# Kernel optimization log

Hardware: AMD Instinct MI355X
Metric: run time of the kernel (lower is better)

Reference implementation:

```python
import jax, jax.numpy as jnp
import numpy as np

N_NODES = 10000
N_EDGES = 640000
EMB_DIM = 128
NUM_RELS = 500


def setup_inputs() -> dict:
    key = jax.random.key(0)
    k_h, k_s, k_d, k_e, k_f, k_r = jax.random.split(key, 6)
    h = jax.random.normal(k_h, (N_NODES, EMB_DIM), dtype=jnp.float32)
    src = jax.random.randint(k_s, (N_EDGES,), 0, N_NODES, dtype=jnp.int64)
    dst = jax.random.randint(k_d, (N_EDGES,), 0, N_NODES, dtype=jnp.int64)
    etype = jax.random.randint(k_e, (N_EDGES,), 0, NUM_RELS, dtype=jnp.int64)
    fwd_rel = jax.random.normal(k_f, (NUM_RELS, EMB_DIM), dtype=jnp.float32)
    rev_rel = jax.random.normal(k_r, (NUM_RELS, EMB_DIM), dtype=jnp.float32)
    return {"h": h, "src": src, "dst": dst, "etype": etype,
            "fwd_rel": fwd_rel, "rev_rel": rev_rel}


def reference(h, src, dst, etype, fwd_rel, rev_rel):
    # DistMult forward-direction scoring (num_rels > 1 branch):
    #   w  = fwd_rel[etype]                  -> [E, D]
    #   ht = h[src] * w                      (u_mul_e)
    #   score[e] = <ht[e], h[dst[e]]>        (e_dot_v)
    w = fwd_rel[etype]                       # [E, D] gather
    h_u = h[src]                             # [E, D] gather
    h_v = h[dst]                             # [E, D] gather
    score = jnp.einsum("ed,ed,ed->e", h_u, w, h_v)  # [E]
    return score
```

## Files before the change

### kernel.cpp

```cpp
#include <hip/hip_runtime.h>
#include <hip/hip_fp16.h>


typedef unsigned short u16;

constexpr int EMB_DIM  = 128;
constexpr int MAX_RELS = 500;
constexpr int BLOCKS   = 256;
constexpr int THREADS  = 1024;

__global__ __launch_bounds__(256) void convert_fp16_kernel(
    const float* __restrict__ a, u16* __restrict__ a16, int n_a8,
    const float* __restrict__ b, u16* __restrict__ b16, int n_b8)
{
    const int total = n_a8 + n_b8;
    for (int i = blockIdx.x * blockDim.x + threadIdx.x; i < total;
         i += gridDim.x * blockDim.x) {
        const float* s; u16* d; int j;
        if (i < n_a8) { s = a; d = a16; j = i; }
        else          { s = b; d = b16; j = i - n_a8; }
        float4 lo = reinterpret_cast<const float4*>(s)[j * 2];
        float4 hi = reinterpret_cast<const float4*>(s)[j * 2 + 1];
        u16 u0 = __half_as_ushort(__float2half(lo.x));
        u16 u1 = __half_as_ushort(__float2half(lo.y));
        u16 u2 = __half_as_ushort(__float2half(lo.z));
        u16 u3 = __half_as_ushort(__float2half(lo.w));
        u16 u4 = __half_as_ushort(__float2half(hi.x));
        u16 u5 = __half_as_ushort(__float2half(hi.y));
        u16 u6 = __half_as_ushort(__float2half(hi.z));
        u16 u7 = __half_as_ushort(__float2half(hi.w));
        uint4 v;
        v.x = (unsigned)u0 | ((unsigned)u1 << 16);
        v.y = (unsigned)u2 | ((unsigned)u3 << 16);
        v.z = (unsigned)u4 | ((unsigned)u5 << 16);
        v.w = (unsigned)u6 | ((unsigned)u7 << 16);
        reinterpret_cast<uint4*>(d)[j] = v;
    }
}

__device__ __forceinline__ float dot8(uint4 A, uint4 B, uint4 C) {
    const __half2* a2 = reinterpret_cast<const __half2*>(&A);
    const __half2* b2 = reinterpret_cast<const __half2*>(&B);
    const __half2* c2 = reinterpret_cast<const __half2*>(&C);
    float acc = 0.f;
    #pragma unroll
    for (int k = 0; k < 4; ++k) {
        float2 fa = __half22float2(a2[k]);
        float2 fb = __half22float2(b2[k]);
        float2 fc = __half22float2(c2[k]);
        acc += fa.x * fb.x * fc.x + fa.y * fb.y * fc.y;
    }
    return acc;
}

__global__ __launch_bounds__(THREADS) void distmult_fp16_kernel(
    const u16* __restrict__ h16,
    const int* __restrict__ src,
    const int* __restrict__ dst,
    const int* __restrict__ etype,
    const u16* __restrict__ w16,
    float*     __restrict__ out,
    int n_edges, int n_rels)
{
    __shared__ u16 w_lds[MAX_RELS * EMB_DIM];

    {
        const int slots = n_rels * (EMB_DIM / 8);
        for (int s = threadIdx.x; s < slots; s += THREADS)
            reinterpret_cast<uint4*>(w_lds)[s] =
                reinterpret_cast<const uint4*>(w16)[s];
    }
    __syncthreads();

    const int team = threadIdx.x >> 4;
    const int lane = threadIdx.x & 15;

    const uint4* hp = reinterpret_cast<const uint4*>(h16) + lane;
    const uint4* wl = reinterpret_cast<const uint4*>(w_lds) + lane;

    const int stride = BLOCKS * (THREADS / 16) * 4;

    for (int e0 = (blockIdx.x * (THREADS / 16) + team) * 4; e0 < n_edges;
         e0 += stride) {
        if (e0 + 3 < n_edges) {
            const int4 s4 = *reinterpret_cast<const int4*>(src   + e0);
            const int4 d4 = *reinterpret_cast<const int4*>(dst   + e0);
            const int4 t4 = *reinterpret_cast<const int4*>(etype + e0);

            uint4 a0 = hp[(size_t)s4.x * 16];
            uint4 a1 = hp[(size_t)s4.y * 16];
            uint4 a2 = hp[(size_t)s4.z * 16];
            uint4 a3 = hp[(size_t)s4.w * 16];
            uint4 c0 = hp[(size_t)d4.x * 16];
            uint4 c1 = hp[(size_t)d4.y * 16];
            uint4 c2 = hp[(size_t)d4.z * 16];
            uint4 c3 = hp[(size_t)d4.w * 16];
            uint4 b0 = wl[(size_t)t4.x * 16];
            uint4 b1 = wl[(size_t)t4.y * 16];
            uint4 b2 = wl[(size_t)t4.z * 16];
            uint4 b3 = wl[(size_t)t4.w * 16];

            float acc0 = dot8(a0, b0, c0);
            float acc1 = dot8(a1, b1, c1);
            float acc2 = dot8(a2, b2, c2);
            float acc3 = dot8(a3, b3, c3);

            #pragma unroll
            for (int off = 8; off > 0; off >>= 1) {
                acc0 += __shfl_down(acc0, off, 16);
                acc1 += __shfl_down(acc1, off, 16);
                acc2 += __shfl_down(acc2, off, 16);
                acc3 += __shfl_down(acc3, off, 16);
            }
            if (lane == 0)
                *reinterpret_cast<float4*>(out + e0) =
                    make_float4(acc0, acc1, acc2, acc3);
        } else {
            for (int k = 0; k < 4; ++k) {
                const int e = e0 + k;
                if (e >= n_edges) break;
                uint4 a = hp[(size_t)src[e] * 16];
                uint4 c = hp[(size_t)dst[e] * 16];
                uint4 b = wl[(size_t)etype[e] * 16];
                float acc = dot8(a, b, c);
                #pragma unroll
                for (int off = 8; off > 0; off >>= 1)
                    acc += __shfl_down(acc, off, 16);
                if (lane == 0) out[e] = acc;
            }
        }
    }
}

__global__ __launch_bounds__(256) void distmult_score_kernel(
    const float* __restrict__ h,
    const int*   __restrict__ src,
    const int*   __restrict__ dst,
    const int*   __restrict__ etype,
    const float* __restrict__ fwd_rel,
    float*       __restrict__ out,
    int n_edges)
{
    const int tid  = blockIdx.x * blockDim.x + threadIdx.x;
    const int lane = threadIdx.x & 63;
    const int half = lane >> 5;
    const int sub  = lane & 31;
    const int edge = (tid >> 6) * 2 + half;
    if (edge >= n_edges) return;

    const int s = src[edge];
    const int d = dst[edge];
    const int e = etype[edge];

    const float4 a = reinterpret_cast<const float4*>(h       + (size_t)s * EMB_DIM)[sub];
    const float4 b = reinterpret_cast<const float4*>(fwd_rel + (size_t)e * EMB_DIM)[sub];
    const float4 c = reinterpret_cast<const float4*>(h       + (size_t)d * EMB_DIM)[sub];

    float acc = a.x*b.x*c.x + a.y*b.y*c.y + a.z*b.z*c.z + a.w*b.w*c.w;
    #pragma unroll
    for (int off = 16; off > 0; off >>= 1)
        acc += __shfl_down(acc, off, 32);
    if (sub == 0) out[edge] = acc;
}

extern "C" void kernel_launch(void* const* d_in, const int* in_sizes, int n_in,
                              void* d_out, int out_size, void* d_ws, size_t ws_size,
                              hipStream_t stream) {
    const float* h       = (const float*)d_in[0];
    const int*   src     = (const int*)d_in[1];
    const int*   dst     = (const int*)d_in[2];
    const int*   etype   = (const int*)d_in[3];
    const float* fwd_rel = (const float*)d_in[4];
    float* out = (float*)d_out;

    const int n_edges = in_sizes[1];
    const int n_h     = in_sizes[0];
    const int n_w     = in_sizes[4];
    const int n_rels  = n_w / EMB_DIM;
    const size_t need = (size_t)(n_h + n_w) * sizeof(u16);

    if (ws_size >= need && n_rels <= MAX_RELS &&
        (n_h % 8) == 0 && (n_w % 8) == 0) {
        u16* h16 = (u16*)d_ws;
        u16* w16 = h16 + n_h;

        const int n_a8 = n_h / 8, n_b8 = n_w / 8;
        const int cgrid = (n_a8 + n_b8 + 255) / 256;
        convert_fp16_kernel<<<cgrid, 256, 0, stream>>>(
            h, h16, n_a8, fwd_rel, w16, n_b8);

        distmult_fp16_kernel<<<BLOCKS, THREADS, 0, stream>>>(
            h16, src, dst, etype, w16, out, n_edges, n_rels);
    } else {
        const int grid = (n_edges + 7) / 8;
        distmult_score_kernel<<<grid, 256, 0, stream>>>(
            h, src, dst, etype, fwd_rel, out, n_edges);
    }
}
```

Measured before the change: 93.59 us.

## Fuse fp16 conversion into scoring kernel via cooperative grid sync and prefetch indices

Folds the fp32-to-fp16 conversion of node embeddings and relation table into the scoring kernel, using a cooperative launch with a grid-wide sync to remove the separate conversion launch. The edge loop now software-prefetches the next iteration's src/dst/etype indices, and the per-edge dot product multiplies a and c in packed fp16 before converting to float. If the cooperative launch fails, it falls back to two launches. Risks include grid-sync overhead, occupancy limits with 1024-thread blocks and large LDS use, and extra fp16 rounding from the packed product.

```diff
diff --git a/kernel.cpp b/kernel.cpp
--- a/kernel.cpp
+++ b/kernel.cpp
@@ -1,13 +1,37 @@
 #include <hip/hip_runtime.h>
 #include <hip/hip_fp16.h>
+#include <hip/hip_cooperative_groups.h>
 
 
 typedef unsigned short u16;
+typedef _Float16 h2v __attribute__((ext_vector_type(2)));
 
 constexpr int EMB_DIM  = 128;
 constexpr int MAX_RELS = 500;
 constexpr int BLOCKS   = 256;
 constexpr int THREADS  = 1024;
+
+namespace cg = cooperative_groups;
+
+__device__ __forceinline__ void convert_slot(const float* __restrict__ s,
+                                             u16* __restrict__ d, int j) {
+    float4 lo = reinterpret_cast<const float4*>(s)[j * 2];
+    float4 hi = reinterpret_cast<const float4*>(s)[j * 2 + 1];
+    u16 u0 = __half_as_ushort(__float2half(lo.x));
+    u16 u1 = __half_as_ushort(__float2half(lo.y));
+    u16 u2 = __half_as_ushort(__float2half(lo.z));
+    u16 u3 = __half_as_ushort(__float2half(lo.w));
+    u16 u4 = __half_as_ushort(__float2half(hi.x));
+    u16 u5 = __half_as_ushort(__float2half(hi.y));
+    u16 u6 = __half_as_ushort(__float2half(hi.z));
+    u16 u7 = __half_as_ushort(__float2half(hi.w));
+    uint4 v;
+    v.x = (unsigned)u0 | ((unsigned)u1 << 16);
+    v.y = (unsigned)u2 | ((unsigned)u3 << 16);
+    v.z = (unsigned)u4 | ((unsigned)u5 << 16);
+    v.w = (unsigned)u6 | ((unsigned)u7 << 16);
+    reinterpret_cast<uint4*>(d)[j] = v;
+}
 
 __global__ __launch_bounds__(256) void convert_fp16_kernel(
     const float* __restrict__ a, u16* __restrict__ a16, int n_a8,
@@ -16,54 +40,46 @@
     const int total = n_a8 + n_b8;
     for (int i = blockIdx.x * blockDim.x + threadIdx.x; i < total;
          i += gridDim.x * blockDim.x) {
-        const float* s; u16* d; int j;
-        if (i < n_a8) { s = a; d = a16; j = i; }
-        else          { s = b; d = b16; j = i - n_a8; }
-        float4 lo = reinterpret_cast<const float4*>(s)[j * 2];
-        float4 hi = reinterpret_cast<const float4*>(s)[j * 2 + 1];
-        u16 u0 = __half_as_ushort(__float2half(lo.x));
-        u16 u1 = __half_as_ushort(__float2half(lo.y));
-        u16 u2 = __half_as_ushort(__float2half(lo.z));
-        u16 u3 = __half_as_ushort(__float2half(lo.w));
-        u16 u4 = __half_as_ushort(__float2half(hi.x));
-        u16 u5 = __half_as_ushort(__float2half(hi.y));
-        u16 u6 = __half_as_ushort(__float2half(hi.z));
-        u16 u7 = __half_as_ushort(__float2half(hi.w));
-        uint4 v;
-        v.x = (unsigned)u0 | ((unsigned)u1 << 16);
-        v.y = (unsigned)u2 | ((unsigned)u3 << 16);
-        v.z = (unsigned)u4 | ((unsigned)u5 << 16);
-        v.w = (unsigned)u6 | ((unsigned)u7 << 16);
-        reinterpret_cast<uint4*>(d)[j] = v;
-    }
-}
-
-__device__ __forceinline__ float dot8(uint4 A, uint4 B, uint4 C) {
-    const __half2* a2 = reinterpret_cast<const __half2*>(&A);
-    const __half2* b2 = reinterpret_cast<const __half2*>(&B);
-    const __half2* c2 = reinterpret_cast<const __half2*>(&C);
-    float acc = 0.f;
+        if (i < n_a8) convert_slot(a, a16, i);
+        else          convert_slot(b, b16, i - n_a8);
+    }
+}
+
+__device__ __forceinline__ float dot8(uint4 A, uint4 B, uint4 C, float acc) {
+    const h2v* a = reinterpret_cast<const h2v*>(&A);
+    const h2v* b = reinterpret_cast<const h2v*>(&B);
+    const h2v* c = reinterpret_cast<const h2v*>(&C);
     #pragma unroll
     for (int k = 0; k < 4; ++k) {
-        float2 fa = __half22float2(a2[k]);
-        float2 fb = __half22float2(b2[k]);
-        float2 fc = __half22float2(c2[k]);
-        acc += fa.x * fb.x * fc.x + fa.y * fb.y * fc.y;
+        h2v t = a[k] * c[k];
+        acc += (float)t.x * (float)b[k].x;
+        acc += (float)t.y * (float)b[k].y;
     }
     return acc;
 }
 
-__global__ __launch_bounds__(THREADS) void distmult_fp16_kernel(
-    const u16* __restrict__ h16,
-    const int* __restrict__ src,
-    const int* __restrict__ dst,
-    const int* __restrict__ etype,
-    const u16* __restrict__ w16,
-    float*     __restrict__ out,
-    int n_edges, int n_rels)
+__global__ __launch_bounds__(THREADS) void distmult_fused_kernel(
+    const float* __restrict__ hf,
+    const float* __restrict__ wf,
+    u16*         __restrict__ h16,
+    u16*         __restrict__ w16,
+    const int*   __restrict__ src,
+    const int*   __restrict__ dst,
+    const int*   __restrict__ etype,
+    float*       __restrict__ out,
+    int n_h8, int n_w8, int n_edges, int n_rels, int do_convert)
 {
+    if (do_convert) {
+        const int total = n_h8 + n_w8;
+        for (int i = blockIdx.x * blockDim.x + threadIdx.x; i < total;
+             i += gridDim.x * blockDim.x) {
+            if (i < n_h8) convert_slot(hf, h16, i);
+            else          convert_slot(wf, w16, i - n_h8);
+        }
+        cg::this_grid().sync();
+    }
+
     __shared__ u16 w_lds[MAX_RELS * EMB_DIM];
-
     {
         const int slots = n_rels * (EMB_DIM / 8);
         for (int s = threadIdx.x; s < slots; s += THREADS)
@@ -80,55 +96,66 @@
 
     const int stride = BLOCKS * (THREADS / 16) * 4;
 
-    for (int e0 = (blockIdx.x * (THREADS / 16) + team) * 4; e0 < n_edges;
-         e0 += stride) {
-        if (e0 + 3 < n_edges) {
-            const int4 s4 = *reinterpret_cast<const int4*>(src   + e0);
-            const int4 d4 = *reinterpret_cast<const int4*>(dst   + e0);
-            const int4 t4 = *reinterpret_cast<const int4*>(etype + e0);
-
-            uint4 a0 = hp[(size_t)s4.x * 16];
-            uint4 a1 = hp[(size_t)s4.y * 16];
-            uint4 a2 = hp[(size_t)s4.z * 16];
-            uint4 a3 = hp[(size_t)s4.w * 16];
-            uint4 c0 = hp[(size_t)d4.x * 16];
-            uint4 c1 = hp[(size_t)d4.y * 16];
-            uint4 c2 = hp[(size_t)d4.z * 16];
-            uint4 c3 = hp[(size_t)d4.w * 16];
-            uint4 b0 = wl[(size_t)t4.x * 16];
-            uint4 b1 = wl[(size_t)t4.y * 16];
-            uint4 b2 = wl[(size_t)t4.z * 16];
-            uint4 b3 = wl[(size_t)t4.w * 16];
-
-            float acc0 = dot8(a0, b0, c0);
-            float acc1 = dot8(a1, b1, c1);
-            float acc2 = dot8(a2, b2, c2);
-            float acc3 = dot8(a3, b3, c3);
-
-            #pragma unroll
-            for (int off = 8; off > 0; off >>= 1) {
-                acc0 += __shfl_down(acc0, off, 16);
-                acc1 += __shfl_down(acc1, off, 16);
-                acc2 += __shfl_down(acc2, off, 16);
-                acc3 += __shfl_down(acc3, off, 16);
-            }
-            if (lane == 0)
-                *reinterpret_cast<float4*>(out + e0) =
-                    make_float4(acc0, acc1, acc2, acc3);
-        } else {
-            for (int k = 0; k < 4; ++k) {
-                const int e = e0 + k;
-                if (e >= n_edges) break;
-                uint4 a = hp[(size_t)src[e] * 16];
-                uint4 c = hp[(size_t)dst[e] * 16];
-                uint4 b = wl[(size_t)etype[e] * 16];
-                float acc = dot8(a, b, c);
-                #pragma unroll
-                for (int off = 8; off > 0; off >>= 1)
-                    acc += __shfl_down(acc, off, 16);
-                if (lane == 0) out[e] = acc;
-            }
-        }
+    int e0 = (blockIdx.x * (THREADS / 16) + team) * 4;
+    int4 s4, d4, t4;
+    bool valid = (e0 + 3 < n_edges);
+    if (valid) {
+        s4 = *reinterpret_cast<const int4*>(src   + e0);
+        d4 = *reinterpret_cast<const int4*>(dst   + e0);
+        t4 = *reinterpret_cast<const int4*>(etype + e0);
+    }
+
+    while (valid) {
+        const int e1 = e0 + stride;
+        const bool nvalid = (e1 + 3 < n_edges);
+        int4 ns = s4, nd = d4, nt = t4;
+        if (nvalid) {
+            ns = *reinterpret_cast<const int4*>(src   + e1);
+            nd = *reinterpret_cast<const int4*>(dst   + e1);
+            nt = *reinterpret_cast<const int4*>(etype + e1);
+        }
+
+        const uint4 a0 = hp[(size_t)(unsigned)s4.x * 16];
+        const uint4 a1 = hp[(size_t)(unsigned)s4.y * 16];
+        const uint4 a2 = hp[(size_t)(unsigned)s4.z * 16];
+        const uint4 a3 = hp[(size_t)(unsigned)s4.w * 16];
+        const uint4 c0 = hp[(size_t)(unsigned)d4.x * 16];
+        const uint4 c1 = hp[(size_t)(unsigned)d4.y * 16];
+        const uint4 c2 = hp[(size_t)(unsigned)d4.z * 16];
+        const uint4 c3 = hp[(size_t)(unsigned)d4.w * 16];
+        const uint4 b0 = wl[(unsigned)t4.x * 16];
+        const uint4 b1 = wl[(unsigned)t4.y * 16];
+        const uint4 b2 = wl[(unsigned)t4.z * 16];
+        const uint4 b3 = wl[(unsigned)t4.w * 16];
+
+        float acc0 = dot8(a0, b0, c0, 0.f);
+        float acc1 = dot8(a1, b1, c1, 0.f);
+        float acc2 = dot8(a2, b2, c2, 0.f);
+        float acc3 = dot8(a3, b3, c3, 0.f);
+
+        #pragma unroll
+        for (int off = 8; off > 0; off >>= 1) {
+            acc0 += __shfl_down(acc0, off, 16);
+            acc1 += __shfl_down(acc1, off, 16);
+            acc2 += __shfl_down(acc2, off, 16);
+            acc3 += __shfl_down(acc3, off, 16);
+        }
+        if (lane == 0)
+            *reinterpret_cast<float4*>(out + e0) =
+                make_float4(acc0, acc1, acc2, acc3);
+
+        e0 = e1; s4 = ns; d4 = nd; t4 = nt; valid = nvalid;
+    }
+
+    for (int e = e0; e < n_edges && e < e0 + 4; ++e) {
+        const uint4 a = hp[(size_t)(unsigned)src[e]   * 16];
+        const uint4 c = hp[(size_t)(unsigned)dst[e]   * 16];
+        const uint4 b = wl[(unsigned)etype[e] * 16];
+        float acc = dot8(a, b, c, 0.f);
+        #pragma unroll
+        for (int off = 8; off > 0; off >>= 1)
+            acc += __shfl_down(acc, off, 16);
+        if (lane == 0) out[e] = acc;
     }
 }
 
@@ -183,14 +210,26 @@
         (n_h % 8) == 0 && (n_w % 8) == 0) {
         u16* h16 = (u16*)d_ws;
         u16* w16 = h16 + n_h;
-
-        const int n_a8 = n_h / 8, n_b8 = n_w / 8;
-        const int cgrid = (n_a8 + n_b8 + 255) / 256;
-        convert_fp16_kernel<<<cgrid, 256, 0, stream>>>(
-            h, h16, n_a8, fwd_rel, w16, n_b8);
-
-        distmult_fp16_kernel<<<BLOCKS, THREADS, 0, stream>>>(
-            h16, src, dst, etype, w16, out, n_edges, n_rels);
+        int n_h8 = n_h / 8, n_w8 = n_w / 8;
+        int ne = n_edges, nr = n_rels, do_conv = 1;
+        const float* hf = h; const float* wf = fwd_rel;
+        const int* sp = src; const int* dp = dst; const int* tp = etype;
+        float* op = out;
+
+        void* args[] = { &hf, &wf, &h16, &w16, &sp, &dp, &tp, &op,
+                         &n_h8, &n_w8, &ne, &nr, &do_conv };
+        hipError_t err = hipLaunchCooperativeKernel(
+            (const void*)distmult_fused_kernel, dim3(BLOCKS), dim3(THREADS),
+            args, 0, stream);
+
+        if (err != hipSuccess) {
+            const int cgrid = (n_h8 + n_w8 + 255) / 256;
+            convert_fp16_kernel<<<cgrid, 256, 0, stream>>>(
+                h, h16, n_h8, fwd_rel, w16, n_w8);
+            distmult_fused_kernel<<<BLOCKS, THREADS, 0, stream>>>(
+                h, fwd_rel, h16, w16, src, dst, etype, out,
+                n_h8, n_w8, n_edges, n_rels, 0);
+        }
     } else {
         const int grid = (n_edges + 7) / 8;
         distmult_score_kernel<<<grid, 256, 0, stream>>>(
```

New measurement: 146.4 us. 1.56x slower.

## Process eight edges per team with prefetched indices and packed fp16 multiply

Applied to the files above, without the earlier changes.

Each 16-lane team now handles eight edges per iteration instead of four, and the next iteration's src/dst/etype indices are loaded before the current gathers so index latency overlaps with row fetches. The dot product uses a packed fp16 multiply of h[src] and h[dst] before widening to float, and the launch bounds add a minimum-occupancy hint. The aim is more memory-level parallelism in the gather loop at the cost of higher register pressure and slightly lower accuracy from the fp16 intermediate product.

```diff
diff --git a/kernel.cpp b/kernel.cpp
--- a/kernel.cpp
+++ b/kernel.cpp
@@ -3,11 +3,33 @@
 
 
 typedef unsigned short u16;
+typedef _Float16 h2v __attribute__((ext_vector_type(2)));
 
 constexpr int EMB_DIM  = 128;
 constexpr int MAX_RELS = 500;
 constexpr int BLOCKS   = 256;
 constexpr int THREADS  = 1024;
+constexpr int EPT      = 8;
+
+__device__ __forceinline__ void convert_slot(const float* __restrict__ s,
+                                             u16* __restrict__ d, int j) {
+    float4 lo = reinterpret_cast<const float4*>(s)[j * 2];
+    float4 hi = reinterpret_cast<const float4*>(s)[j * 2 + 1];
+    u16 u0 = __half_as_ushort(__float2half(lo.x));
+    u16 u1 = __half_as_ushort(__float2half(lo.y));
+    u16 u2 = __half_as_ushort(__float2half(lo.z));
+    u16 u3 = __half_as_ushort(__float2half(lo.w));
+    u16 u4 = __half_as_ushort(__float2half(hi.x));
+    u16 u5 = __half_as_ushort(__float2half(hi.y));
+    u16 u6 = __half_as_ushort(__float2half(hi.z));
+    u16 u7 = __half_as_ushort(__float2half(hi.w));
+    uint4 v;
+    v.x = (unsigned)u0 | ((unsigned)u1 << 16);
+    v.y = (unsigned)u2 | ((unsigned)u3 << 16);
+    v.z = (unsigned)u4 | ((unsigned)u5 << 16);
+    v.w = (unsigned)u6 | ((unsigned)u7 << 16);
+    reinterpret_cast<uint4*>(d)[j] = v;
+}
 
 __global__ __launch_bounds__(256) void convert_fp16_kernel(
     const float* __restrict__ a, u16* __restrict__ a16, int n_a8,
@@ -16,44 +38,33 @@
     const int total = n_a8 + n_b8;
     for (int i = blockIdx.x * blockDim.x + threadIdx.x; i < total;
          i += gridDim.x * blockDim.x) {
-        const float* s; u16* d; int j;
-        if (i < n_a8) { s = a; d = a16; j = i; }
-        else          { s = b; d = b16; j = i - n_a8; }
-        float4 lo = reinterpret_cast<const float4*>(s)[j * 2];
-        float4 hi = reinterpret_cast<const float4*>(s)[j * 2 + 1];
-        u16 u0 = __half_as_ushort(__float2half(lo.x));
-        u16 u1 = __half_as_ushort(__float2half(lo.y));
-        u16 u2 = __half_as_ushort(__float2half(lo.z));
-        u16 u3 = __half_as_ushort(__float2half(lo.w));
-        u16 u4 = __half_as_ushort(__float2half(hi.x));
-        u16 u5 = __half_as_ushort(__float2half(hi.y));
-        u16 u6 = __half_as_ushort(__float2half(hi.z));
-        u16 u7 = __half_as_ushort(__float2half(hi.w));
-        uint4 v;
-        v.x = (unsigned)u0 | ((unsigned)u1 << 16);
-        v.y = (unsigned)u2 | ((unsigned)u3 << 16);
-        v.z = (unsigned)u4 | ((unsigned)u5 << 16);
-        v.w = (unsigned)u6 | ((unsigned)u7 << 16);
-        reinterpret_cast<uint4*>(d)[j] = v;
+        if (i < n_a8) convert_slot(a, a16, i);
+        else          convert_slot(b, b16, i - n_a8);
     }
 }
 
 __device__ __forceinline__ float dot8(uint4 A, uint4 B, uint4 C) {
-    const __half2* a2 = reinterpret_cast<const __half2*>(&A);
-    const __half2* b2 = reinterpret_cast<const __half2*>(&B);
-    const __half2* c2 = reinterpret_cast<const __half2*>(&C);
+    const h2v* a = reinterpret_cast<const h2v*>(&A);
+    const h2v* b = reinterpret_cast<const h2v*>(&B);
+    const h2v* c = reinterpret_cast<const h2v*>(&C);
     float acc = 0.f;
     #pragma unroll
     for (int k = 0; k < 4; ++k) {
-        float2 fa = __half22float2(a2[k]);
-        float2 fb = __half22float2(b2[k]);
-        float2 fc = __half22float2(c2[k]);
-        acc += fa.x * fb.x * fc.x + fa.y * fb.y * fc.y;
+        h2v t = a[k] * c[k];
+        acc += (float)t.x * (float)b[k].x;
+        acc += (float)t.y * (float)b[k].y;
     }
     return acc;
 }
 
-__global__ __launch_bounds__(THREADS) void distmult_fp16_kernel(
+__device__ __forceinline__ float team_reduce16(float acc) {
+    #pragma unroll
+    for (int off = 8; off > 0; off >>= 1)
+        acc += __shfl_down(acc, off, 16);
+    return acc;
+}
+
+__global__ __launch_bounds__(THREADS, 4) void distmult_fp16_kernel(
     const u16* __restrict__ h16,
     const int* __restrict__ src,
     const int* __restrict__ dst,
@@ -78,57 +89,95 @@
     const uint4* hp = reinterpret_cast<const uint4*>(h16) + lane;
     const uint4* wl = reinterpret_cast<const uint4*>(w_lds) + lane;
 
-    const int stride = BLOCKS * (THREADS / 16) * 4;
-
-    for (int e0 = (blockIdx.x * (THREADS / 16) + team) * 4; e0 < n_edges;
-         e0 += stride) {
-        if (e0 + 3 < n_edges) {
-            const int4 s4 = *reinterpret_cast<const int4*>(src   + e0);
-            const int4 d4 = *reinterpret_cast<const int4*>(dst   + e0);
-            const int4 t4 = *reinterpret_cast<const int4*>(etype + e0);
-
-            uint4 a0 = hp[(size_t)s4.x * 16];
-            uint4 a1 = hp[(size_t)s4.y * 16];
-            uint4 a2 = hp[(size_t)s4.z * 16];
-            uint4 a3 = hp[(size_t)s4.w * 16];
-            uint4 c0 = hp[(size_t)d4.x * 16];
-            uint4 c1 = hp[(size_t)d4.y * 16];
-            uint4 c2 = hp[(size_t)d4.z * 16];
-            uint4 c3 = hp[(size_t)d4.w * 16];
-            uint4 b0 = wl[(size_t)t4.x * 16];
-            uint4 b1 = wl[(size_t)t4.y * 16];
-            uint4 b2 = wl[(size_t)t4.z * 16];
-            uint4 b3 = wl[(size_t)t4.w * 16];
-
-            float acc0 = dot8(a0, b0, c0);
-            float acc1 = dot8(a1, b1, c1);
-            float acc2 = dot8(a2, b2, c2);
-            float acc3 = dot8(a3, b3, c3);
-
-            #pragma unroll
-            for (int off = 8; off > 0; off >>= 1) {
-                acc0 += __shfl_down(acc0, off, 16);
-                acc1 += __shfl_down(acc1, off, 16);
-                acc2 += __shfl_down(acc2, off, 16);
-                acc3 += __shfl_down(acc3, off, 16);
-            }
-            if (lane == 0)
-                *reinterpret_cast<float4*>(out + e0) =
-                    make_float4(acc0, acc1, acc2, acc3);
-        } else {
-            for (int k = 0; k < 4; ++k) {
-                const int e = e0 + k;
-                if (e >= n_edges) break;
-                uint4 a = hp[(size_t)src[e] * 16];
-                uint4 c = hp[(size_t)dst[e] * 16];
-                uint4 b = wl[(size_t)etype[e] * 16];
-                float acc = dot8(a, b, c);
-                #pragma unroll
-                for (int off = 8; off > 0; off >>= 1)
-                    acc += __shfl_down(acc, off, 16);
-                if (lane == 0) out[e] = acc;
-            }
+    const int stride = BLOCKS * (THREADS / 16) * EPT;
+
+    int e0 = (blockIdx.x * (THREADS / 16) + team) * EPT;
+    int4 s0v, s1v, d0v, d1v, t0v, t1v;
+    bool valid = (e0 + EPT <= n_edges);
+    if (valid) {
+        s0v = *reinterpret_cast<const int4*>(src   + e0);
+        s1v = *reinterpret_cast<const int4*>(src   + e0 + 4);
+        d0v = *reinterpret_cast<const int4*>(dst   + e0);
+        d1v = *reinterpret_cast<const int4*>(dst   + e0 + 4);
+        t0v = *reinterpret_cast<const int4*>(etype + e0);
+        t1v = *reinterpret_cast<const int4*>(etype + e0 + 4);
+    }
+
+    while (valid) {
+        const int e1 = e0 + stride;
+        const bool nvalid = (e1 + EPT <= n_edges);
+        int4 ns0 = s0v, ns1 = s1v, nd0 = d0v, nd1 = d1v, nt0 = t0v, nt1 = t1v;
+        if (nvalid) {
+            ns0 = *reinterpret_cast<const int4*>(src   + e1);
+            ns1 = *reinterpret_cast<const int4*>(src   + e1 + 4);
+            nd0 = *reinterpret_cast<const int4*>(dst   + e1);
+            nd1 = *reinterpret_cast<const int4*>(dst   + e1 + 4);
+            nt0 = *reinterpret_cast<const int4*>(etype + e1);
+            nt1 = *reinterpret_cast<const int4*>(etype + e1 + 4);
         }
+
+        const uint4 a0 = hp[(size_t)(unsigned)s0v.x * 16];
+        const uint4 a1 = hp[(size_t)(unsigned)s0v.y * 16];
+        const uint4 a2 = hp[(size_t)(unsigned)s0v.z * 16];
+        const uint4 a3 = hp[(size_t)(unsigned)s0v.w * 16];
+        const uint4 a4 = hp[(size_t)(unsigned)s1v.x * 16];
+        const uint4 a5 = hp[(size_t)(unsigned)s1v.y * 16];
+        const uint4 a6 = hp[(size_t)(unsigned)s1v.z * 16];
+        const uint4 a7 = hp[(size_t)(unsigned)s1v.w * 16];
+        const uint4 c0 = hp[(size_t)(unsigned)d0v.x * 16];
+        const uint4 c1 = hp[(size_t)(unsigned)d0v.y * 16];
+        const uint4 c2 = hp[(size_t)(unsigned)d0v.z * 16];
+        const uint4 c3 = hp[(size_t)(unsigned)d0v.w * 16];
+        const uint4 c4 = hp[(size_t)(unsigned)d1v.x * 16];
+        const uint4 c5 = hp[(size_t)(unsigned)d1v.y * 16];
+        const uint4 c6 = hp[(size_t)(unsigned)d1v.z * 16];
+        const uint4 c7 = hp[(size_t)(unsigned)d1v.w * 16];
+
+        const uint4 b0 = wl[(unsigned)t0v.x * 16];
+        const uint4 b1 = wl[(unsigned)t0v.y * 16];
+        const uint4 b2 = wl[(unsigned)t0v.z * 16];
+        const uint4 b3 = wl[(unsigned)t0v.w * 16];
+        float acc0 = dot8(a0, b0, c0);
+        float acc1 = dot8(a1, b1, c1);
+        float acc2 = dot8(a2, b2, c2);
+        float acc3 = dot8(a3, b3, c3);
+
+        const uint4 b4 = wl[(unsigned)t1v.x * 16];
+        const uint4 b5 = wl[(unsigned)t1v.y * 16];
+        const uint4 b6 = wl[(unsigned)t1v.z * 16];
+        const uint4 b7 = wl[(unsigned)t1v.w * 16];
+        float acc4 = dot8(a4, b4, c4);
+        float acc5 = dot8(a5, b5, c5);
+        float acc6 = dot8(a6, b6, c6);
+        float acc7 = dot8(a7, b7, c7);
+
+        acc0 = team_reduce16(acc0);
+        acc1 = team_reduce16(acc1);
+        acc2 = team_reduce16(acc2);
+        acc3 = team_reduce16(acc3);
+        acc4 = team_reduce16(acc4);
+        acc5 = team_reduce16(acc5);
+        acc6 = team_reduce16(acc6);
+        acc7 = team_reduce16(acc7);
+
+        if (lane == 0) {
+            *reinterpret_cast<float4*>(out + e0) =
+                make_float4(acc0, acc1, acc2, acc3);
+            *reinterpret_cast<float4*>(out + e0 + 4) =
+                make_float4(acc4, acc5, acc6, acc7);
+        }
+
+        e0 = e1;
+        s0v = ns0; s1v = ns1; d0v = nd0; d1v = nd1; t0v = nt0; t1v = nt1;
+        valid = nvalid;
+    }
+
+    for (int e = e0; e < n_edges && e < e0 + EPT; ++e) {
+        const uint4 a = hp[(size_t)(unsigned)src[e]   * 16];
+        const uint4 c = hp[(size_t)(unsigned)dst[e]   * 16];
+        const uint4 b = wl[(unsigned)etype[e] * 16];
+        float acc = team_reduce16(dot8(a, b, c));
+        if (lane == 0) out[e] = acc;
     }
 }
 
```

After: 133.8 us. 1.43x slower.
